# Optimization experiments

Hardware: AMD Instinct MI355X
Metric: run time of the kernel (lower is better)

The kernel has to match this reference:

```python
import jax, jax.numpy as jnp
import numpy as np

CUTOFF = 5.0
N_ATOMS, N_EDGES, D, R = 100000, 1600000, 64, 20


def setup_inputs() -> dict:
    key = jax.random.key(0)
    ks = jax.random.split(key, 12)
    ve = jax.random.normal(ks[0], (N_ATOMS, D, 3), dtype=jnp.float32)
    se = jax.random.normal(ks[1], (N_ATOMS, D), dtype=jnp.float32)
    dirs = jax.random.normal(ks[2], (N_EDGES, 3), dtype=jnp.float32)
    dirs = dirs / jnp.linalg.norm(dirs, axis=-1, keepdims=True)
    dist = jax.random.uniform(ks[3], (N_EDGES,), minval=0.5, maxval=CUTOFF, dtype=jnp.float32)
    nv = dirs * dist[:, None]  # neighbour_vectors with norm in (0.5, cutoff)
    central = jax.random.randint(ks[4], (N_EDGES,), 0, N_ATOMS)
    neigh = jax.random.randint(ks[5], (N_EDGES,), 0, N_ATOMS)
    # Bessel frequencies n*pi/cutoff (learnable in graph-pes)
    freqs = (jnp.arange(1, R + 1, dtype=jnp.float32) * np.pi / CUTOFF)
    W_filter = jax.random.normal(ks[6], (R, 3 * D), dtype=jnp.float32) / np.sqrt(R)
    b_filter = jnp.zeros((3 * D,), dtype=jnp.float32)
    W1 = jax.random.normal(ks[7], (D, D), dtype=jnp.float32) / np.sqrt(D)
    b1 = jnp.zeros((D,), dtype=jnp.float32)
    W2 = jax.random.normal(ks[8], (D, 3 * D), dtype=jnp.float32) / np.sqrt(D)
    b2 = jnp.zeros((3 * D,), dtype=jnp.float32)
    return {
        'vector_embeddings': ve, 'scalar_embeddings': se, 'neighbour_vectors': nv,
        'central_atoms': central, 'neighbours': neigh,
        'freqs': freqs, 'W_filter': W_filter, 'b_filter': b_filter,
        'W1': W1, 'b1': b1, 'W2': W2, 'b2': b2,
    }


def _envelope(d):
    # polynomial envelope, p = 6
    u = d / CUTOFF
    env = 1.0 - 28.0 * u**6 + 48.0 * u**7 - 21.0 * u**8
    return jnp.where(d < CUTOFF, env, 0.0)


def reference(vector_embeddings, scalar_embeddings, neighbour_vectors,
              central_atoms, neighbours, freqs, W_filter, b_filter,
              W1, b1, W2, b2):
    d = jnp.linalg.norm(neighbour_vectors, axis=-1)                 # [E]
    unit = neighbour_vectors / d[:, None]                           # [E, 3]
    # Bessel radial basis: sqrt(2/c) * sin(f_n d) / d
    bessel = np.sqrt(2.0 / CUTOFF) * jnp.sin(freqs[None, :] * d[:, None]) / d[:, None]  # [E, R]
    filt = (bessel @ W_filter + b_filter) * _envelope(d)[:, None]   # [E, 3D]
    # phi: MLP [D, D, 3D] with SiLU between layers
    h = jax.nn.silu(scalar_embeddings @ W1 + b1) @ W2 + b2          # [N, 3D]
    x_ij = filt * h[central_atoms]                                  # [E, 3D]
    a, b, c = jnp.split(x_ij, 3, axis=-1)                           # each [E, D]
    n = scalar_embeddings.shape[0]
    delta_s = jax.ops.segment_sum(a, neighbours, num_segments=n)    # [N, D]
    v_ij = b[:, :, None] * unit[:, None, :] + c[:, :, None] * vector_embeddings[neighbours]  # [E, D, 3]
    delta_v = jax.ops.segment_sum(v_ij, neighbours, num_segments=n)  # [N, D, 3]
    return (delta_v, delta_s)
```

## Files before the change

### kernel.cpp

```cpp
#include <hip/hip_runtime.h>
#include <math.h>

#define DCH 64
#define TD 192
#define RR 20
#define FCUT 5.0f

typedef __attribute__((ext_vector_type(8))) short short8;
typedef __attribute__((ext_vector_type(4))) float f32x4;
typedef __attribute__((ext_vector_type(2))) unsigned int u32x2;

__device__ __forceinline__ unsigned short f2bf(float f) {
    unsigned int u = __float_as_uint(f);
    u += 0x7FFFu + ((u >> 16) & 1u);
    return (unsigned short)(u >> 16);
}
__device__ __forceinline__ float bflo(unsigned int u) {
    return __uint_as_float(u << 16);
}
__device__ __forceinline__ float bfhi(unsigned int u) {
    return __uint_as_float(u & 0xFFFF0000u);
}

__global__ __launch_bounds__(256, 2) void mlp_mfma_kernel(
    const float* __restrict__ se,
    const float* __restrict__ W1, const float* __restrict__ b1,
    const float* __restrict__ W2, const float* __restrict__ b2,
    unsigned short* __restrict__ h2, int N)
{
    const int wid  = threadIdx.x >> 6;
    const int lane = threadIdx.x & 63;
    const int g    = lane >> 4;
    const int c    = lane & 15;

    __shared__ float hmid[4][16][68];
    __shared__ unsigned short hstage[4][16][196];

    short8 W1f[4][2];
    float  b1t[4];
    #pragma unroll
    for (int t = 0; t < 4; ++t) {
        #pragma unroll
        for (int kh = 0; kh < 2; ++kh)
            #pragma unroll
            for (int j = 0; j < 8; ++j) {
                int k = kh * 32 + 8 * g + j;
                W1f[t][kh][j] = (short)f2bf(W1[k * DCH + 16 * t + c]);
            }
        b1t[t] = b1[16 * t + c];
    }
    short8 W2f[12][2];
    float  b2t[12];
    #pragma unroll
    for (int t = 0; t < 12; ++t) {
        #pragma unroll
        for (int kh = 0; kh < 2; ++kh)
            #pragma unroll
            for (int j = 0; j < 8; ++j) {
                int k = kh * 32 + 8 * g + j;
                W2f[t][kh][j] = (short)f2bf(W2[k * TD + 16 * t + c]);
            }
        b2t[t] = b2[16 * t + c];
    }

    for (int base = blockIdx.x * 64; base < N; base += gridDim.x * 64) {
        const int arow = base + wid * 16;
        const int atom = arow + c;
        const bool va  = atom < N;

        const float* sp = se + (size_t)(va ? atom : 0) * DCH;
        short8 A0, A1;
        #pragma unroll
        for (int kh = 0; kh < 2; ++kh) {
            f32x4 q0 = va ? __builtin_nontemporal_load((const f32x4*)(sp + kh*32 + 8*g))
                          : (f32x4){0.f,0.f,0.f,0.f};
            f32x4 q1 = va ? __builtin_nontemporal_load((const f32x4*)(sp + kh*32 + 8*g + 4))
                          : (f32x4){0.f,0.f,0.f,0.f};
            short8& A = kh ? A1 : A0;
            A[0] = (short)f2bf(q0[0]); A[1] = (short)f2bf(q0[1]);
            A[2] = (short)f2bf(q0[2]); A[3] = (short)f2bf(q0[3]);
            A[4] = (short)f2bf(q1[0]); A[5] = (short)f2bf(q1[1]);
            A[6] = (short)f2bf(q1[2]); A[7] = (short)f2bf(q1[3]);
        }

        #pragma unroll
        for (int t = 0; t < 4; ++t) {
            f32x4 C = {0.f, 0.f, 0.f, 0.f};
            C = __builtin_amdgcn_mfma_f32_16x16x32_bf16(A0, W1f[t][0], C, 0, 0, 0);
            C = __builtin_amdgcn_mfma_f32_16x16x32_bf16(A1, W1f[t][1], C, 0, 0, 0);
            #pragma unroll
            for (int reg = 0; reg < 4; ++reg) {
                float x = C[reg] + b1t[t];
                float s = x / (1.0f + __expf(-x));
                hmid[wid][4 * g + reg][16 * t + c] = s;
            }
        }
        __syncthreads();

        short8 B0, B1;
        #pragma unroll
        for (int kh = 0; kh < 2; ++kh) {
            const float* hp = &hmid[wid][c][kh * 32 + 8 * g];
            f32x4 q0 = *(const f32x4*)(hp);
            f32x4 q1 = *(const f32x4*)(hp + 4);
            short8& A = kh ? B1 : B0;
            A[0] = (short)f2bf(q0[0]); A[1] = (short)f2bf(q0[1]);
            A[2] = (short)f2bf(q0[2]); A[3] = (short)f2bf(q0[3]);
            A[4] = (short)f2bf(q1[0]); A[5] = (short)f2bf(q1[1]);
            A[6] = (short)f2bf(q1[2]); A[7] = (short)f2bf(q1[3]);
        }

        #pragma unroll
        for (int t = 0; t < 12; ++t) {
            f32x4 C = {0.f, 0.f, 0.f, 0.f};
            C = __builtin_amdgcn_mfma_f32_16x16x32_bf16(B0, W2f[t][0], C, 0, 0, 0);
            C = __builtin_amdgcn_mfma_f32_16x16x32_bf16(B1, W2f[t][1], C, 0, 0, 0);
            #pragma unroll
            for (int reg = 0; reg < 4; ++reg)
                hstage[wid][4 * g + reg][c * 12 + t] = f2bf(C[reg] + b2t[t]);
        }
        __syncthreads();

        if (lane < 48) {
            #pragma unroll
            for (int i = 0; i < 16; ++i) {
                int a2 = arow + i;
                if (a2 < N)
                    *(u32x2*)((char*)h2 + (size_t)a2 * 384 + lane * 8) =
                        *(const u32x2*)(&hstage[wid][i][lane * 4]);
            }
        }
    }
}

__global__ void hist_kernel(const int* __restrict__ neigh,
                            int* __restrict__ counts, int* __restrict__ pos, int E)
{
    int stride = gridDim.x * blockDim.x;
    for (int e = blockIdx.x * blockDim.x + threadIdx.x; e < E; e += stride) {
        int p = atomicAdd(&counts[neigh[e]], 1);
        __builtin_nontemporal_store(p, &pos[e]);
    }
}

__global__ __launch_bounds__(256) void scan1_kernel(
    const int* __restrict__ counts, int* __restrict__ starts,
    int* __restrict__ bsums, int N)
{
    int tid = threadIdx.x;
    int gid = blockIdx.x * 256 + tid;
    int v = (gid < N) ? counts[gid] : 0;
    int lane = tid & 63, wid = tid >> 6;
    int x = v;
    #pragma unroll
    for (int off = 1; off < 64; off <<= 1) {
        int y = __shfl_up(x, off, 64);
        if (lane >= off) x += y;
    }
    __shared__ int wsum[4];
    if (lane == 63) wsum[wid] = x;
    __syncthreads();
    int add = 0;
    for (int w = 0; w < wid; ++w) add += wsum[w];
    int incl = x + add;
    if (gid < N) starts[gid] = incl - v;
    if (tid == 255) bsums[blockIdx.x] = incl;
}

__global__ __launch_bounds__(512) void scan2_kernel(int* __restrict__ bsums, int M)
{
    int tid = threadIdx.x;
    int v = (tid < M) ? bsums[tid] : 0;
    int lane = tid & 63, wid = tid >> 6;
    int x = v;
    #pragma unroll
    for (int off = 1; off < 64; off <<= 1) {
        int y = __shfl_up(x, off, 64);
        if (lane >= off) x += y;
    }
    __shared__ int wsum[8];
    if (lane == 63) wsum[wid] = x;
    __syncthreads();
    int add = 0;
    for (int w = 0; w < wid; ++w) add += wsum[w];
    int incl = x + add;
    if (tid < M) bsums[tid] = incl - v;
}

__global__ __launch_bounds__(256) void scan3_kernel(
    int* __restrict__ starts, const int* __restrict__ bsums, int N)
{
    int gid = blockIdx.x * 256 + threadIdx.x;
    if (gid < N) starts[gid] += bsums[blockIdx.x];
}

__global__ void fill_kernel(const float* __restrict__ nv, const int* __restrict__ central,
                            const int* __restrict__ neigh, const int* __restrict__ starts,
                            const int* __restrict__ pos, f32x4* __restrict__ payload, int E)
{
    int stride = gridDim.x * blockDim.x;
    for (int e = blockIdx.x * blockDim.x + threadIdx.x; e < E; e += stride) {
        int slot = starts[neigh[e]] + pos[e];
        f32x4 pay;
        pay[0] = __builtin_nontemporal_load(&nv[(size_t)e*3+0]);
        pay[1] = __builtin_nontemporal_load(&nv[(size_t)e*3+1]);
        pay[2] = __builtin_nontemporal_load(&nv[(size_t)e*3+2]);
        pay[3] = __int_as_float(central[e]);
        __builtin_nontemporal_store(pay, &payload[slot]);
    }
}

__global__ __launch_bounds__(256) void gather_kernel(
    const f32x4* __restrict__ payload, const int* __restrict__ starts,
    const int* __restrict__ counts, const unsigned short* __restrict__ h2,
    const float* __restrict__ ve, const float* __restrict__ Wf,
    const float* __restrict__ bfil,
    float* __restrict__ dv, float* __restrict__ ds, int N)
{
    const int wid  = threadIdx.x >> 6;
    const int lane = threadIdx.x & 63;
    const int g    = lane >> 4;
    const int c    = lane & 15;

    short8 Bf[12];
    #pragma unroll
    for (int t = 0; t < 12; ++t) {
        #pragma unroll
        for (int j = 0; j < 8; ++j) {
            int r = 8 * g + j;
            float w = (r < RR) ? Wf[r * TD + 16 * t + c]
                               : (r == RR ? bfil[16 * t + c] : 0.0f);
            Bf[t][j] = (short)f2bf(w);
        }
    }

    const float BC = sqrtf(2.0f / FCUT);
    const float XK = (float)(M_PI / (double)FCUT);
    const char* hb = (const char*)h2;

    for (int atom = blockIdx.x * 4 + wid; atom < N; atom += gridDim.x * 4) {
        const int s   = starts[atom];
        const int cnt = counts[atom];

        float dsa[4] = {0,0,0,0};
        float csm[4] = {0,0,0,0};
        float dvx[4] = {0,0,0,0};
        float dvy[4] = {0,0,0,0};
        float dvz[4] = {0,0,0,0};

        for (int i0 = 0; i0 < cnt; i0 += 16) {
            const bool valid = (i0 + c) < cnt;
            f32x4 p = valid ? __builtin_nontemporal_load(&payload[s + i0 + c])
                            : (f32x4){1.0f, 0.0f, 0.0f, 0.0f};
            float dist = sqrtf(p[0]*p[0] + p[1]*p[1] + p[2]*p[2]);
            float inv  = 1.0f / dist;
            float xa   = dist * XK;

            float u  = dist * (1.0f / FCUT);
            float u2 = u * u;
            float u6 = u2 * u2 * u2;
            float env = 1.0f + u6 * (-28.0f + u * (48.0f - 21.0f * u));
            env = (dist < FCUT && valid) ? env : 0.0f;
            float scale = BC * inv * env;

            float ux = p[0] * inv, uy = p[1] * inv, uz = p[2] * inv;
            int   ca  = valid ? __float_as_int(p[3]) : 0;
            int   hof = ca * 384;

            float bas[8];
            bas[0] = __sinf((float)(8 * g + 1) * xa);
            bas[1] = __sinf((float)(8 * g + 2) * xa);
            float twoc = 2.0f * __cosf(xa);
            #pragma unroll
            for (int j = 2; j < 8; ++j)
                bas[j] = fmaf(twoc, bas[j-1], -bas[j-2]);

            short8 A;
            #pragma unroll
            for (int j = 0; j < 8; ++j)
                A[j] = (short)f2bf(bas[j] * scale);
            if (g == 2) A[4] = (short)f2bf(env);

            float ux_r[4], uy_r[4], uz_r[4];
            int   hof_r[4];
            #pragma unroll
            for (int reg = 0; reg < 4; ++reg) {
                int src = 4 * g + reg;
                ux_r[reg]  = __shfl(ux,  src, 64);
                uy_r[reg]  = __shfl(uy,  src, 64);
                uz_r[reg]  = __shfl(uz,  src, 64);
                hof_r[reg] = __shfl(hof, src, 64);
            }

            u32x2 hq[4][3];
            #pragma unroll
            for (int reg = 0; reg < 4; ++reg) {
                const char* rp = hb + (size_t)(unsigned)hof_r[reg] + c * 24;
                hq[reg][0] = *(const u32x2*)(rp);
                hq[reg][1] = *(const u32x2*)(rp + 8);
                hq[reg][2] = *(const u32x2*)(rp + 16);
            }

            #pragma unroll
            for (int t = 0; t < 12; ++t) {
                f32x4 C = __builtin_amdgcn_mfma_f32_16x16x32_bf16(
                    A, Bf[t], (f32x4){0.f,0.f,0.f,0.f}, 0, 0, 0);
                #pragma unroll
                for (int reg = 0; reg < 4; ++reg) {
                    unsigned int w = hq[reg][t >> 2][(t >> 1) & 1];
                    float hv = (t & 1) ? bfhi(w) : bflo(w);
                    if (t < 4) {
                        dsa[t] = fmaf(C[reg], hv, dsa[t]);
                    } else if (t < 8) {
                        float bh = C[reg] * hv;
                        dvx[t-4] = fmaf(bh, ux_r[reg], dvx[t-4]);
                        dvy[t-4] = fmaf(bh, uy_r[reg], dvy[t-4]);
                        dvz[t-4] = fmaf(bh, uz_r[reg], dvz[t-4]);
                    } else {
                        csm[t-8] = fmaf(C[reg], hv, csm[t-8]);
                    }
                }
            }
        }

        #pragma unroll
        for (int t = 0; t < 4; ++t) {
            dsa[t] += __shfl_xor(dsa[t], 16, 64); dsa[t] += __shfl_xor(dsa[t], 32, 64);
            csm[t] += __shfl_xor(csm[t], 16, 64); csm[t] += __shfl_xor(csm[t], 32, 64);
            dvx[t] += __shfl_xor(dvx[t], 16, 64); dvx[t] += __shfl_xor(dvx[t], 32, 64);
            dvy[t] += __shfl_xor(dvy[t], 16, 64); dvy[t] += __shfl_xor(dvy[t], 32, 64);
            dvz[t] += __shfl_xor(dvz[t], 16, 64); dvz[t] += __shfl_xor(dvz[t], 32, 64);
        }

        float dssel = (g==0) ? dsa[0] : (g==1) ? dsa[1] : (g==2) ? dsa[2] : dsa[3];
        float cssel = (g==0) ? csm[0] : (g==1) ? csm[1] : (g==2) ? csm[2] : csm[3];
        float vxsel = (g==0) ? dvx[0] : (g==1) ? dvx[1] : (g==2) ? dvx[2] : dvx[3];
        float vysel = (g==0) ? dvy[0] : (g==1) ? dvy[1] : (g==2) ? dvy[2] : dvy[3];
        float vzsel = (g==0) ? dvz[0] : (g==1) ? dvz[1] : (g==2) ? dvz[2] : dvz[3];

        int ch = 16 * g + c;
        size_t vb = (size_t)atom * TD + (size_t)ch * 3;
        float v0 = __builtin_nontemporal_load(&ve[vb + 0]);
        float v1 = __builtin_nontemporal_load(&ve[vb + 1]);
        float v2 = __builtin_nontemporal_load(&ve[vb + 2]);
        __builtin_nontemporal_store(fmaf(cssel, v0, vxsel), &dv[vb + 0]);
        __builtin_nontemporal_store(fmaf(cssel, v1, vysel), &dv[vb + 1]);
        __builtin_nontemporal_store(fmaf(cssel, v2, vzsel), &dv[vb + 2]);
        __builtin_nontemporal_store(dssel, &ds[(size_t)atom * DCH + ch]);
    }
}

extern "C" void kernel_launch(void* const* d_in, const int* in_sizes, int n_in,
                              void* d_out, int out_size, void* d_ws, size_t ws_size,
                              hipStream_t stream) {
    const float* ve      = (const float*)d_in[0];
    const float* se      = (const float*)d_in[1];
    const float* nv      = (const float*)d_in[2];
    const int*   central = (const int*)  d_in[3];
    const int*   neigh   = (const int*)  d_in[4];
    const float* Wf      = (const float*)d_in[6];
    const float* bfil    = (const float*)d_in[7];
    const float* W1      = (const float*)d_in[8];
    const float* b1      = (const float*)d_in[9];
    const float* W2      = (const float*)d_in[10];
    const float* b2      = (const float*)d_in[11];

    const int N = in_sizes[1] / DCH;
    const int E = in_sizes[3];

    float* out = (float*)d_out;
    float* dv  = out;
    float* ds  = out + (size_t)N * TD;

    char* wsb = (char*)d_ws;
    size_t off = 0;
    auto wsalloc = [&](size_t bytes) -> void* {
        void* p = wsb + off;
        off = (off + bytes + 255) & ~(size_t)255;
        return p;
    };
    unsigned short* h2      = (unsigned short*)wsalloc((size_t)N * 192 * 2);
    int*            counts  = (int*)   wsalloc((size_t)N * 4);
    int*            starts  = (int*)   wsalloc((size_t)N * 4);
    int*            pos     = (int*)   wsalloc((size_t)E * 4);
    f32x4*          payload = (f32x4*) wsalloc((size_t)E * 16);
    int*            bsums   = (int*)   wsalloc(4096);

    const int nb1 = (N + 255) / 256;
    const int nbm = (N + 63) / 64;

    mlp_mfma_kernel<<<nbm, 256, 0, stream>>>(se, W1, b1, W2, b2, h2, N);

    hipMemsetAsync(counts, 0, (size_t)N * 4, stream);
    hist_kernel<<<2048, 256, 0, stream>>>(neigh, counts, pos, E);
    scan1_kernel<<<nb1, 256, 0, stream>>>(counts, starts, bsums, N);
    scan2_kernel<<<1, 512, 0, stream>>>(bsums, nb1);
    scan3_kernel<<<nb1, 256, 0, stream>>>(starts, bsums, N);
    fill_kernel<<<2048, 256, 0, stream>>>(nv, central, neigh, starts, pos, payload, E);
    gather_kernel<<<4096, 256, 0, stream>>>(payload, starts, counts, h2, ve,
                                            Wf, bfil, dv, ds, N);
}
```

Baseline: 370.4 us.

## Software-pipeline payload and h-row gathers across edge chunks in gather kernel

Restructures the per-atom edge loop in the gather kernel into a software pipeline. The h rows for the next 16-edge chunk and the payload two chunks ahead are prefetched while the current chunk does its MFMA work, so that gather latency is hidden. It also switches the bf16 conversion to the HIP intrinsic and halves the gather grid size. The prefetch buffers raise register pressure and may reduce occupancy, and the smaller grid lowers parallelism.

Result: slower. 405.9 us (+9.6%).

```diff
diff --git a/kernel.cpp b/kernel.cpp
--- a/kernel.cpp
+++ b/kernel.cpp
@@ -1,4 +1,5 @@
 #include <hip/hip_runtime.h>
+#include <hip/hip_bf16.h>
 #include <math.h>
 
 #define DCH 64
@@ -14,6 +15,11 @@
     unsigned int u = __float_as_uint(f);
     u += 0x7FFFu + ((u >> 16) & 1u);
     return (unsigned short)(u >> 16);
+}
+__device__ __forceinline__ short f2bfn(float f) {
+    union { __hip_bfloat16 b; short s; } u;
+    u.b = __float2bfloat16(f);
+    return u.s;
 }
 __device__ __forceinline__ float bflo(unsigned int u) {
     return __uint_as_float(u << 16);
@@ -248,77 +254,101 @@
         float dvy[4] = {0,0,0,0};
         float dvz[4] = {0,0,0,0};
 
-        for (int i0 = 0; i0 < cnt; i0 += 16) {
-            const bool valid = (i0 + c) < cnt;
-            f32x4 p = valid ? __builtin_nontemporal_load(&payload[s + i0 + c])
-                            : (f32x4){1.0f, 0.0f, 0.0f, 0.0f};
-            float dist = sqrtf(p[0]*p[0] + p[1]*p[1] + p[2]*p[2]);
-            float inv  = 1.0f / dist;
-            float xa   = dist * XK;
-
-            float u  = dist * (1.0f / FCUT);
-            float u2 = u * u;
-            float u6 = u2 * u2 * u2;
-            float env = 1.0f + u6 * (-28.0f + u * (48.0f - 21.0f * u));
-            env = (dist < FCUT && valid) ? env : 0.0f;
-            float scale = BC * inv * env;
-
-            float ux = p[0] * inv, uy = p[1] * inv, uz = p[2] * inv;
-            int   ca  = valid ? __float_as_int(p[3]) : 0;
-            int   hof = ca * 384;
-
-            float bas[8];
-            bas[0] = __sinf((float)(8 * g + 1) * xa);
-            bas[1] = __sinf((float)(8 * g + 2) * xa);
-            float twoc = 2.0f * __cosf(xa);
-            #pragma unroll
-            for (int j = 2; j < 8; ++j)
-                bas[j] = fmaf(twoc, bas[j-1], -bas[j-2]);
-
-            short8 A;
-            #pragma unroll
-            for (int j = 0; j < 8; ++j)
-                A[j] = (short)f2bf(bas[j] * scale);
-            if (g == 2) A[4] = (short)f2bf(env);
-
-            float ux_r[4], uy_r[4], uz_r[4];
-            int   hof_r[4];
-            #pragma unroll
-            for (int reg = 0; reg < 4; ++reg) {
-                int src = 4 * g + reg;
-                ux_r[reg]  = __shfl(ux,  src, 64);
-                uy_r[reg]  = __shfl(uy,  src, 64);
-                uz_r[reg]  = __shfl(uz,  src, 64);
-                hof_r[reg] = __shfl(hof, src, 64);
-            }
-
-            u32x2 hq[4][3];
-            #pragma unroll
-            for (int reg = 0; reg < 4; ++reg) {
-                const char* rp = hb + (size_t)(unsigned)hof_r[reg] + c * 24;
-                hq[reg][0] = *(const u32x2*)(rp);
-                hq[reg][1] = *(const u32x2*)(rp + 8);
-                hq[reg][2] = *(const u32x2*)(rp + 16);
-            }
-
-            #pragma unroll
-            for (int t = 0; t < 12; ++t) {
-                f32x4 C = __builtin_amdgcn_mfma_f32_16x16x32_bf16(
-                    A, Bf[t], (f32x4){0.f,0.f,0.f,0.f}, 0, 0, 0);
+        if (cnt > 0) {
+            auto loadP = [&](int i0) -> f32x4 {
+                return ((i0 + c) < cnt)
+                    ? __builtin_nontemporal_load(&payload[s + i0 + c])
+                    : (f32x4){1.0f, 0.0f, 0.0f, 0.0f};
+            };
+            auto loadH = [&](const f32x4& p, int i0, u32x2 (&hq)[4][3]) {
+                int ca  = ((i0 + c) < cnt) ? __float_as_int(p[3]) : 0;
+                int hof = ca * 384;
                 #pragma unroll
                 for (int reg = 0; reg < 4; ++reg) {
-                    unsigned int w = hq[reg][t >> 2][(t >> 1) & 1];
-                    float hv = (t & 1) ? bfhi(w) : bflo(w);
-                    if (t < 4) {
-                        dsa[t] = fmaf(C[reg], hv, dsa[t]);
-                    } else if (t < 8) {
-                        float bh = C[reg] * hv;
-                        dvx[t-4] = fmaf(bh, ux_r[reg], dvx[t-4]);
-                        dvy[t-4] = fmaf(bh, uy_r[reg], dvy[t-4]);
-                        dvz[t-4] = fmaf(bh, uz_r[reg], dvz[t-4]);
-                    } else {
-                        csm[t-8] = fmaf(C[reg], hv, csm[t-8]);
+                    int hofr = __shfl(hof, 4 * g + reg, 64);
+                    const char* rp = hb + (size_t)(unsigned)hofr + c * 24;
+                    hq[reg][0] = *(const u32x2*)(rp);
+                    hq[reg][1] = *(const u32x2*)(rp + 8);
+                    hq[reg][2] = *(const u32x2*)(rp + 16);
+                }
+            };
+
+            f32x4 pA = loadP(0);
+            u32x2 hqA[4][3];
+            loadH(pA, 0, hqA);
+            f32x4 pB = (16 < cnt) ? loadP(16) : pA;
+
+            for (int i0 = 0; i0 < cnt; i0 += 16) {
+                const bool has_next = (i0 + 16) < cnt;
+
+                u32x2 hqB[4][3];
+                if (has_next) loadH(pB, i0 + 16, hqB);
+                f32x4 pC = (has_next && (i0 + 32) < cnt) ? loadP(i0 + 32) : pB;
+
+                const bool valid = (i0 + c) < cnt;
+                float dist = sqrtf(pA[0]*pA[0] + pA[1]*pA[1] + pA[2]*pA[2]);
+                float inv  = 1.0f / dist;
+                float xa   = dist * XK;
+
+                float u  = dist * (1.0f / FCUT);
+                float u2 = u * u;
+                float u6 = u2 * u2 * u2;
+                float env = 1.0f + u6 * (-28.0f + u * (48.0f - 21.0f * u));
+                env = (dist < FCUT && valid) ? env : 0.0f;
+                float scale = BC * inv * env;
+
+                float ux = pA[0] * inv, uy = pA[1] * inv, uz = pA[2] * inv;
+
+                float bas[8];
+                bas[0] = __sinf((float)(8 * g + 1) * xa);
+                bas[1] = __sinf((float)(8 * g + 2) * xa);
+                float twoc = 2.0f * __cosf(xa);
+                #pragma unroll
+                for (int j = 2; j < 8; ++j)
+                    bas[j] = fmaf(twoc, bas[j-1], -bas[j-2]);
+
+                short8 A;
+                #pragma unroll
+                for (int j = 0; j < 8; ++j)
+                    A[j] = f2bfn(bas[j] * scale);
+                if (g == 2) A[4] = f2bfn(env);
+
+                float ux_r[4], uy_r[4], uz_r[4];
+                #pragma unroll
+                for (int reg = 0; reg < 4; ++reg) {
+                    int src = 4 * g + reg;
+                    ux_r[reg] = __shfl(ux, src, 64);
+                    uy_r[reg] = __shfl(uy, src, 64);
+                    uz_r[reg] = __shfl(uz, src, 64);
+                }
+
+                #pragma unroll
+                for (int t = 0; t < 12; ++t) {
+                    f32x4 C = __builtin_amdgcn_mfma_f32_16x16x32_bf16(
+                        A, Bf[t], (f32x4){0.f,0.f,0.f,0.f}, 0, 0, 0);
+                    #pragma unroll
+                    for (int reg = 0; reg < 4; ++reg) {
+                        unsigned int w = hqA[reg][t >> 2][(t >> 1) & 1];
+                        float hv = (t & 1) ? bfhi(w) : bflo(w);
+                        if (t < 4) {
+                            dsa[t] = fmaf(C[reg], hv, dsa[t]);
+                        } else if (t < 8) {
+                            float bh = C[reg] * hv;
+                            dvx[t-4] = fmaf(bh, ux_r[reg], dvx[t-4]);
+                            dvy[t-4] = fmaf(bh, uy_r[reg], dvy[t-4]);
+                            dvz[t-4] = fmaf(bh, uz_r[reg], dvz[t-4]);
+                        } else {
+                            csm[t-8] = fmaf(C[reg], hv, csm[t-8]);
+                        }
                     }
+                }
+
+                pA = pB; pB = pC;
+                #pragma unroll
+                for (int reg = 0; reg < 4; ++reg) {
+                    hqA[reg][0] = hqB[reg][0];
+                    hqA[reg][1] = hqB[reg][1];
+                    hqA[reg][2] = hqB[reg][2];
                 }
             }
         }
@@ -397,6 +427,6 @@
     scan2_kernel<<<1, 512, 0, stream>>>(bsums, nb1);
     scan3_kernel<<<nb1, 256, 0, stream>>>(starts, bsums, N);
     fill_kernel<<<2048, 256, 0, stream>>>(nv, central, neigh, starts, pos, payload, E);
-    gather_kernel<<<4096, 256, 0, stream>>>(payload, starts, counts, h2, ve,
+    gather_kernel<<<2048, 256, 0, stream>>>(payload, starts, counts, h2, ve,
                                             Wf, bfil, dv, ds, N);
 }
```
